# Kernel tuning notes

Measured on AMD Instinct MI355X. Metric: run time of the kernel, lower is better.

## Reference

```python
import jax, jax.numpy as jnp
import numpy as np

B, N, D, ATT = 8, 2048, 1024, 128

def setup_inputs() -> dict:
    key = jax.random.key(0)
    k1, k2, k3 = jax.random.split(key, 3)
    s = 1.0 / np.sqrt(D)
    return {
        "x": jax.random.normal(k1, (B, N, D), dtype=jnp.float32),
        "Wf": jax.random.normal(k2, (D, ATT), dtype=jnp.float32) * s,
        "bf": jnp.zeros((ATT,), dtype=jnp.float32),
        "Wg": jax.random.normal(k3, (D, ATT), dtype=jnp.float32) * s,
        "bg": jnp.zeros((ATT,), dtype=jnp.float32),
    }

def reference(x, Wf, bf, Wg, bg):
    # f, g: [B, N, ATT]
    f = jnp.einsum('bnd,da->bna', x, Wf) + bf
    g = jnp.einsum('bnd,da->bna', x, Wg) + bg
    # unscaled attention logits [B, N, N]
    att = jnp.einsum('bna,bma->bnm', f, g)
    att = jax.nn.softmax(att, axis=-1)
    # NOTE: original multiplies attention with x (not h); h branch is dead code.
    out = jnp.einsum('bnm,bmd->bnd', att, x)
    return out + x  # residual=True
```

## Files before the change

### kernel.cpp

```cpp
#include <hip/hip_runtime.h>
#include <hip/hip_fp16.h>


#define B_ 8
#define N_ 2048
#define D_ 1024
#define A_ 128

typedef _Float16 half8v  __attribute__((ext_vector_type(8)));
typedef _Float16 half4v  __attribute__((ext_vector_type(4)));
typedef short    short8v __attribute__((ext_vector_type(8)));
typedef float    floatx4 __attribute__((ext_vector_type(4)));

#define SOFT_C 44.0f

__device__ __forceinline__ floatx4 mfma32(half8v a, half8v b, floatx4 c) {
#if defined(__HIP_DEVICE_COMPILE__)
    return __builtin_amdgcn_mfma_f32_16x16x32_f16(a, b, c, 0, 0, 0);
#else
    return c;
#endif
}
__device__ __forceinline__ floatx4 mfma32bf(short8v a, short8v b, floatx4 c) {
#if defined(__HIP_DEVICE_COMPILE__)
    return __builtin_amdgcn_mfma_f32_16x16x32_bf16(a, b, c, 0, 0, 0);
#else
    return c;
#endif
}

__device__ __forceinline__ unsigned short f2bf(float x) {
    union { float f; unsigned int u; } v; v.f = x;
    unsigned int u = v.u + 0x7fffu + ((v.u >> 16) & 1u);
    return (unsigned short)(u >> 16);
}

__device__ __forceinline__ void gload_lds16(const void* gsrc, void* ldst) {
#if defined(__HIP_DEVICE_COMPILE__)
    __builtin_amdgcn_global_load_lds(
        (const __attribute__((address_space(1))) void*)gsrc,
        (__attribute__((address_space(3))) void*)ldst, 16, 0, 0);
#endif
}

__global__ __launch_bounds__(256) void xpose_kernel(
    const float* __restrict__ x, unsigned short* __restrict__ xT)
{
    __shared__ __align__(16) unsigned short ts[64][80];
    const int n0 = blockIdx.x * 64, d0 = blockIdx.y * 64, b = blockIdx.z;
    const int t = threadIdx.x;
#pragma unroll
    for (int s = 0; s < 4; ++s) {
        int idx = t + 256 * s;
        int nl = idx >> 4, c4 = idx & 15;
        float4 v = ((const float4*)(x + ((size_t)(b * N_ + n0 + nl)) * D_ + d0))[c4];
        ts[c4 * 4 + 0][nl] = f2bf(v.x);
        ts[c4 * 4 + 1][nl] = f2bf(v.y);
        ts[c4 * 4 + 2][nl] = f2bf(v.z);
        ts[c4 * 4 + 3][nl] = f2bf(v.w);
    }
    __syncthreads();
#pragma unroll
    for (int s = 0; s < 2; ++s) {
        int idx = t + 256 * s;
        int dl = idx >> 3, c = idx & 7;
        *(uint4*)&xT[((size_t)b * D_ + d0 + dl) * N_ + n0 + c * 8] =
            *(const uint4*)&ts[dl][c * 8];
    }
}

__global__ __launch_bounds__(256) void wprep_kernel(
    const float* __restrict__ Wf, const float* __restrict__ Wg,
    _Float16* __restrict__ whT)
{
    __shared__ __align__(16) _Float16 ts[64][72];
    const int k0 = blockIdx.x * 64, c0 = blockIdx.y * 64;
    const float* W = blockIdx.z ? Wg : Wf;
    _Float16* dst = whT + (size_t)blockIdx.z * A_ * D_;
    const int t = threadIdx.x;
#pragma unroll
    for (int s = 0; s < 4; ++s) {
        int idx = t + 256 * s;
        int kl = idx >> 4, c4 = idx & 15;
        float4 v = *(const float4*)&W[(size_t)(k0 + kl) * A_ + c0 + c4 * 4];
        ts[c4 * 4 + 0][kl] = (_Float16)v.x;
        ts[c4 * 4 + 1][kl] = (_Float16)v.y;
        ts[c4 * 4 + 2][kl] = (_Float16)v.z;
        ts[c4 * 4 + 3][kl] = (_Float16)v.w;
    }
    __syncthreads();
#pragma unroll
    for (int s = 0; s < 2; ++s) {
        int idx = t + 256 * s;
        int cl = idx >> 3, ch = idx & 7;
        *(uint4*)&dst[(size_t)(c0 + cl) * D_ + k0 + ch * 8] =
            *(const uint4*)&ts[cl][ch * 8];
    }
}

__global__ __launch_bounds__(256) void fgmm_kernel(
    const float* __restrict__ x, const _Float16* __restrict__ whT,
    const float* __restrict__ bfv, const float* __restrict__ bgv,
    _Float16* __restrict__ fh, _Float16* __restrict__ gh)
{
    __shared__ __align__(16) _Float16 xs[64 * 40];
    __shared__ __align__(16) _Float16 wt[256 * 40];
    const int row0 = blockIdx.x * 64;
    const int t = threadIdx.x;
    const int w = t >> 6, lane = t & 63, quad = lane >> 4, l16 = lane & 15;
    const int wr  = (w >> 1) * 32;
    const int wch = (w & 1);

    float4 xRf[2];
    uint4  wR[4];
#define FG_LOAD_TILE(K0)                                                      \
    {                                                                         \
        _Pragma("unroll")                                                     \
        for (int s = 0; s < 2; ++s) {                                         \
            int idx = t + 256 * s;                                            \
            int r = idx >> 3, k4 = idx & 7;                                   \
            xRf[s] = *(const float4*)&x[(size_t)(row0 + r) * D_ + (K0) + k4 * 4]; \
        }                                                                     \
        _Pragma("unroll")                                                     \
        for (int s = 0; s < 4; ++s) {                                         \
            int idx = t + 256 * s;                                            \
            int c = idx >> 2, k8 = idx & 3;                                   \
            wR[s] = *(const uint4*)&whT[(size_t)c * D_ + (K0) + k8 * 8];      \
        }                                                                     \
    }

    FG_LOAD_TILE(0)

    floatx4 acc[2][8];
#pragma unroll
    for (int ms = 0; ms < 2; ++ms)
#pragma unroll
        for (int nt = 0; nt < 8; ++nt)
            acc[ms][nt] = (floatx4){0.f, 0.f, 0.f, 0.f};

    for (int kt = 0; kt < 32; ++kt) {
        __syncthreads();
#pragma unroll
        for (int s = 0; s < 2; ++s) {
            int idx = t + 256 * s;
            int r = idx >> 3, k4 = idx & 7;
            half4v h = {(_Float16)xRf[s].x, (_Float16)xRf[s].y,
                        (_Float16)xRf[s].z, (_Float16)xRf[s].w};
            *(half4v*)&xs[r * 40 + k4 * 4] = h;
        }
#pragma unroll
        for (int s = 0; s < 4; ++s) {
            int idx = t + 256 * s;
            int c = idx >> 2, k8 = idx & 3;
            *(uint4*)&wt[c * 40 + k8 * 8] = wR[s];
        }
        __syncthreads();
        if (kt < 31) FG_LOAD_TILE((kt + 1) * 32)

        half8v a0 = *(const half8v*)&xs[(wr + l16) * 40 + quad * 8];
        half8v a1 = *(const half8v*)&xs[(wr + 16 + l16) * 40 + quad * 8];
#pragma unroll
        for (int nt = 0; nt < 8; ++nt) {
            half8v bfr = *(const half8v*)&wt[(wch * 128 + nt * 16 + l16) * 40 + quad * 8];
            acc[0][nt] = mfma32(a0, bfr, acc[0][nt]);
            acc[1][nt] = mfma32(a1, bfr, acc[1][nt]);
        }
    }

    _Float16* dst = wch ? gh : fh;
    const float* bias = wch ? bgv : bfv;
#pragma unroll
    for (int nt = 0; nt < 8; ++nt) {
        int col = nt * 16 + l16;
        float bv = bias[col];
#pragma unroll
        for (int ms = 0; ms < 2; ++ms)
#pragma unroll
            for (int rg = 0; rg < 4; ++rg) {
                int row = row0 + wr + ms * 16 + quad * 4 + rg;
                dst[(size_t)row * A_ + col] = (_Float16)(acc[ms][nt][rg] + bv);
            }
    }
}

__global__ __launch_bounds__(512) void attp_kernel(
    const _Float16* __restrict__ f, const _Float16* __restrict__ g,
    unsigned short* __restrict__ P, float* __restrict__ lsum)
{
    __shared__ __align__(16) unsigned short tps[8][16 * 56];
    __shared__ float lred[8][16];

    const int tid = threadIdx.x;
    const int wave = tid >> 6, lane = tid & 63;
    const int quad = lane >> 4, l16 = lane & 15;
    const int gp = wave >> 2, qg = wave & 3;
    const int q0 = blockIdx.x * 64;
    const int b  = blockIdx.y;

    half8v fb[4];
#pragma unroll
    for (int kc = 0; kc < 4; ++kc)
        fb[kc] = *(const half8v*)(f +
            ((size_t)(b * N_ + q0 + qg * 16 + l16)) * A_ + kc * 32 + quad * 8);

    unsigned short* slab = &tps[wave][0];
    float l_part = 0.f;

    for (int t = 0; t < 32; ++t) {
        const int m0 = gp * 1024 + t * 32;
        half8v ga0[4], ga1[4];
#pragma unroll
        for (int kc = 0; kc < 4; ++kc) {
            ga0[kc] = *(const half8v*)(g +
                ((size_t)(b * N_ + m0 + l16)) * A_ + kc * 32 + quad * 8);
            ga1[kc] = *(const half8v*)(g +
                ((size_t)(b * N_ + m0 + 16 + l16)) * A_ + kc * 32 + quad * 8);
        }
        floatx4 sc0 = (floatx4){0.f, 0.f, 0.f, 0.f};
        floatx4 sc1 = (floatx4){0.f, 0.f, 0.f, 0.f};
#pragma unroll
        for (int kc = 0; kc < 4; ++kc) {
            sc0 = mfma32(ga0[kc], fb[kc], sc0);
            sc1 = mfma32(ga1[kc], fb[kc], sc1);
        }
        float e0 = __expf(sc0[0] - SOFT_C), e1 = __expf(sc0[1] - SOFT_C);
        float e2 = __expf(sc0[2] - SOFT_C), e3 = __expf(sc0[3] - SOFT_C);
        float e4 = __expf(sc1[0] - SOFT_C), e5 = __expf(sc1[1] - SOFT_C);
        float e6 = __expf(sc1[2] - SOFT_C), e7 = __expf(sc1[3] - SOFT_C);
        l_part += ((e0 + e1) + (e2 + e3)) + ((e4 + e5) + (e6 + e7));
        unsigned int w01 = (unsigned int)f2bf(e0) | ((unsigned int)f2bf(e1) << 16);
        unsigned int w23 = (unsigned int)f2bf(e2) | ((unsigned int)f2bf(e3) << 16);
        unsigned int w45 = (unsigned int)f2bf(e4) | ((unsigned int)f2bf(e5) << 16);
        unsigned int w67 = (unsigned int)f2bf(e6) | ((unsigned int)f2bf(e7) << 16);
        *(unsigned int*)&slab[l16 * 56 + quad * 4]          = w01;
        *(unsigned int*)&slab[l16 * 56 + quad * 4 + 2]      = w23;
        *(unsigned int*)&slab[l16 * 56 + 16 + quad * 4]     = w45;
        *(unsigned int*)&slab[l16 * 56 + 16 + quad * 4 + 2] = w67;
        asm volatile("s_waitcnt lgkmcnt(0)" ::: "memory");
        __builtin_amdgcn_sched_barrier(0);
        uint4 pvv = *(const uint4*)&slab[(lane >> 2) * 56 + (lane & 3) * 8];
        *(uint4*)(P + ((size_t)(b * N_ + q0 + qg * 16 + (lane >> 2))) * N_ +
                  m0 + (lane & 3) * 8) = pvv;
    }

    l_part += __shfl_xor(l_part, 16);
    l_part += __shfl_xor(l_part, 32);
    if (lane < 16) lred[wave][lane] = l_part;
    __syncthreads();
    if (wave < 4 && lane < 16)
        lsum[(size_t)b * N_ + q0 + wave * 16 + lane] =
            lred[wave][lane] + lred[wave + 4][lane];
}

__global__ __launch_bounds__(256, 4) void pv_kernel(
    const unsigned short* __restrict__ P, const unsigned short* __restrict__ xT,
    const float* __restrict__ lsum, const float* __restrict__ x,
    float* __restrict__ out)
{
    __shared__ __align__(16) unsigned short Ps[2][128 * 32];
    __shared__ __align__(16) unsigned short Xs[2][128 * 32];

    const int bm = blockIdx.x;
    const int dn = blockIdx.y;
    const int b  = blockIdx.z;
    const int tid = threadIdx.x;
    const int wave = tid >> 6, lane = tid & 63;
    const int quad = lane >> 4, l16 = lane & 15;
    const int wm = wave >> 1, wn = wave & 1;
    const int xorv = (l16 >> 1) & 3;
    const int chq = (quad ^ xorv) * 8;

#define PV_STAGE(BUF, T0)                                                     \
    {                                                                         \
        _Pragma("unroll")                                                     \
        for (int s = 0; s < 2; ++s) {                                         \
            int idx = s * 256 + tid;                                          \
            int row = idx >> 2, c = idx & 3;                                  \
            int cc = c ^ ((row >> 1) & 3);                                    \
            gload_lds16(P + ((size_t)(b * N_ + bm * 128 + row)) * N_ +        \
                            (T0) + cc * 8,                                    \
                        &Ps[BUF][(s * 256 + wave * 64) * 8]);                 \
        }                                                                     \
        _Pragma("unroll")                                                     \
        for (int s = 0; s < 2; ++s) {                                         \
            int idx = s * 256 + tid;                                          \
            int row = idx >> 2, c = idx & 3;                                  \
            int cc = c ^ ((row >> 1) & 3);                                    \
            gload_lds16(xT + ((size_t)(b * D_ + dn * 128 + row)) * N_ +       \
                            (T0) + cc * 8,                                    \
                        &Xs[BUF][(s * 256 + wave * 64) * 8]);                 \
        }                                                                     \
    }

    floatx4 acc[4][4];
#pragma unroll
    for (int m = 0; m < 4; ++m)
#pragma unroll
        for (int n = 0; n < 4; ++n)
            acc[m][n] = (floatx4){0.f, 0.f, 0.f, 0.f};

    PV_STAGE(0, 0)
    __syncthreads();

    for (int t = 0; t < 64; ++t) {
        const int cur = t & 1;
        if (t < 63) PV_STAGE(cur ^ 1, (t + 1) * 32)

        short8v a[4], bb[4];
#pragma unroll
        for (int m = 0; m < 4; ++m)
            a[m] = *(const short8v*)&Ps[cur][(wm * 64 + m * 16 + l16) * 32 + chq];
#pragma unroll
        for (int n = 0; n < 4; ++n)
            bb[n] = *(const short8v*)&Xs[cur][(wn * 64 + n * 16 + l16) * 32 + chq];

        __builtin_amdgcn_s_setprio(1);
#pragma unroll
        for (int m = 0; m < 4; ++m)
#pragma unroll
            for (int n = 0; n < 4; ++n)
                acc[m][n] = mfma32bf(a[m], bb[n], acc[m][n]);
        __builtin_amdgcn_s_setprio(0);

        __syncthreads();
    }

    float linv[4][4];
#pragma unroll
    for (int m = 0; m < 4; ++m)
#pragma unroll
        for (int rg = 0; rg < 4; ++rg) {
            int row = bm * 128 + wm * 64 + m * 16 + quad * 4 + rg;
            linv[m][rg] = 1.0f / lsum[(size_t)b * N_ + row];
        }
#pragma unroll
    for (int m = 0; m < 4; ++m)
#pragma unroll
        for (int rg = 0; rg < 4; ++rg) {
            int row = bm * 128 + wm * 64 + m * 16 + quad * 4 + rg;
            const size_t rowoff = ((size_t)(b * N_ + row)) * D_ + dn * 128;
#pragma unroll
            for (int n = 0; n < 4; ++n) {
                int col = wn * 64 + n * 16 + l16;
                out[rowoff + col] =
                    fmaf(acc[m][n][rg], linv[m][rg], x[rowoff + col]);
            }
        }
}

extern "C" void kernel_launch(void* const* d_in, const int* in_sizes, int n_in,
                              void* d_out, int out_size, void* d_ws, size_t ws_size,
                              hipStream_t stream) {
    const float* x   = (const float*)d_in[0];
    const float* Wf  = (const float*)d_in[1];
    const float* bfv = (const float*)d_in[2];
    const float* Wg  = (const float*)d_in[3];
    const float* bgv = (const float*)d_in[4];
    float* out = (float*)d_out;

    _Float16*       fh  = (_Float16*)d_ws;
    _Float16*       gh  = fh + (size_t)B_ * N_ * A_;
    unsigned short* xT  = (unsigned short*)(gh + (size_t)B_ * N_ * A_);
    _Float16*       whT = (_Float16*)(xT + (size_t)B_ * D_ * N_);
    unsigned short* P   = (unsigned short*)(whT + (size_t)2 * A_ * D_);
    float*          lsum = (float*)(P + (size_t)B_ * N_ * N_);

    hipLaunchKernelGGL(xpose_kernel, dim3(N_ / 64, D_ / 64, B_), dim3(256), 0, stream,
                       x, xT);
    hipLaunchKernelGGL(wprep_kernel, dim3(D_ / 64, A_ / 64, 2), dim3(256), 0, stream,
                       Wf, Wg, whT);
    hipLaunchKernelGGL(fgmm_kernel, dim3(B_ * N_ / 64), dim3(256), 0, stream,
                       x, whT, bfv, bgv, fh, gh);
    hipLaunchKernelGGL(attp_kernel, dim3(N_ / 64, B_), dim3(512), 0, stream,
                       fh, gh, P, lsum);
    hipLaunchKernelGGL(pv_kernel, dim3(N_ / 128, D_ / 128, B_), dim3(256), 0, stream,
                       P, xT, lsum, x, out);
}
```

Baseline: 321.7 us.

## Triple-buffer PV loads with vmcnt waits and re-split attention-P grid

The pv_kernel moves from double to triple buffering of LDS tiles. It prefetches two stages ahead and replaces __syncthreads with explicit vmcnt/lgkmcnt waits plus s_barrier, so global loads overlap more with MFMA work. The attp_kernel now uses 256-thread blocks covering 16 query rows, with each wave handling a 512-key slice, and software-prefetches g tiles with ping-pong registers. In exchange it uses more LDS in pv_kernel, lowers its occupancy hint to 3, and launches more attp blocks.

Result: slower. 339.4 us (+5.5%).

```diff
diff --git a/kernel.cpp b/kernel.cpp
--- a/kernel.cpp
+++ b/kernel.cpp
@@ -183,82 +183,96 @@
     }
 }
 
-__global__ __launch_bounds__(512) void attp_kernel(
+__global__ __launch_bounds__(256) void attp_kernel(
     const _Float16* __restrict__ f, const _Float16* __restrict__ g,
     unsigned short* __restrict__ P, float* __restrict__ lsum)
 {
-    __shared__ __align__(16) unsigned short tps[8][16 * 56];
-    __shared__ float lred[8][16];
+    __shared__ __align__(16) unsigned short tps[4][16 * 56];
+    __shared__ float lred[4][16];
 
     const int tid = threadIdx.x;
     const int wave = tid >> 6, lane = tid & 63;
     const int quad = lane >> 4, l16 = lane & 15;
-    const int gp = wave >> 2, qg = wave & 3;
-    const int q0 = blockIdx.x * 64;
+    const int q0 = blockIdx.x * 16;
     const int b  = blockIdx.y;
+    const int kbase = wave * 512;
 
     half8v fb[4];
 #pragma unroll
     for (int kc = 0; kc < 4; ++kc)
         fb[kc] = *(const half8v*)(f +
-            ((size_t)(b * N_ + q0 + qg * 16 + l16)) * A_ + kc * 32 + quad * 8);
+            ((size_t)(b * N_ + q0 + l16)) * A_ + kc * 32 + quad * 8);
 
     unsigned short* slab = &tps[wave][0];
     float l_part = 0.f;
 
-    for (int t = 0; t < 32; ++t) {
-        const int m0 = gp * 1024 + t * 32;
-        half8v ga0[4], ga1[4];
-#pragma unroll
-        for (int kc = 0; kc < 4; ++kc) {
-            ga0[kc] = *(const half8v*)(g +
-                ((size_t)(b * N_ + m0 + l16)) * A_ + kc * 32 + quad * 8);
-            ga1[kc] = *(const half8v*)(g +
-                ((size_t)(b * N_ + m0 + 16 + l16)) * A_ + kc * 32 + quad * 8);
-        }
-        floatx4 sc0 = (floatx4){0.f, 0.f, 0.f, 0.f};
-        floatx4 sc1 = (floatx4){0.f, 0.f, 0.f, 0.f};
-#pragma unroll
-        for (int kc = 0; kc < 4; ++kc) {
-            sc0 = mfma32(ga0[kc], fb[kc], sc0);
-            sc1 = mfma32(ga1[kc], fb[kc], sc1);
-        }
-        float e0 = __expf(sc0[0] - SOFT_C), e1 = __expf(sc0[1] - SOFT_C);
-        float e2 = __expf(sc0[2] - SOFT_C), e3 = __expf(sc0[3] - SOFT_C);
-        float e4 = __expf(sc1[0] - SOFT_C), e5 = __expf(sc1[1] - SOFT_C);
-        float e6 = __expf(sc1[2] - SOFT_C), e7 = __expf(sc1[3] - SOFT_C);
-        l_part += ((e0 + e1) + (e2 + e3)) + ((e4 + e5) + (e6 + e7));
-        unsigned int w01 = (unsigned int)f2bf(e0) | ((unsigned int)f2bf(e1) << 16);
-        unsigned int w23 = (unsigned int)f2bf(e2) | ((unsigned int)f2bf(e3) << 16);
-        unsigned int w45 = (unsigned int)f2bf(e4) | ((unsigned int)f2bf(e5) << 16);
-        unsigned int w67 = (unsigned int)f2bf(e6) | ((unsigned int)f2bf(e7) << 16);
-        *(unsigned int*)&slab[l16 * 56 + quad * 4]          = w01;
-        *(unsigned int*)&slab[l16 * 56 + quad * 4 + 2]      = w23;
-        *(unsigned int*)&slab[l16 * 56 + 16 + quad * 4]     = w45;
-        *(unsigned int*)&slab[l16 * 56 + 16 + quad * 4 + 2] = w67;
-        asm volatile("s_waitcnt lgkmcnt(0)" ::: "memory");
-        __builtin_amdgcn_sched_barrier(0);
-        uint4 pvv = *(const uint4*)&slab[(lane >> 2) * 56 + (lane & 3) * 8];
-        *(uint4*)(P + ((size_t)(b * N_ + q0 + qg * 16 + (lane >> 2))) * N_ +
-                  m0 + (lane & 3) * 8) = pvv;
+#define ATTP_LOADG(A0, A1, M0)                                                \
+    {                                                                         \
+        _Pragma("unroll")                                                     \
+        for (int kc = 0; kc < 4; ++kc) {                                      \
+            A0[kc] = *(const half8v*)(g +                                     \
+                ((size_t)(b * N_ + (M0) + l16)) * A_ + kc * 32 + quad * 8);   \
+            A1[kc] = *(const half8v*)(g +                                     \
+                ((size_t)(b * N_ + (M0) + 16 + l16)) * A_ + kc * 32 + quad * 8); \
+        }                                                                     \
+    }
+
+#define ATTP_COMPUTE(A0, A1, TT)                                              \
+    {                                                                         \
+        const int m0 = kbase + (TT) * 32;                                     \
+        floatx4 sc0 = (floatx4){0.f, 0.f, 0.f, 0.f};                          \
+        floatx4 sc1 = (floatx4){0.f, 0.f, 0.f, 0.f};                          \
+        _Pragma("unroll")                                                     \
+        for (int kc = 0; kc < 4; ++kc) {                                      \
+            sc0 = mfma32(A0[kc], fb[kc], sc0);                                \
+            sc1 = mfma32(A1[kc], fb[kc], sc1);                                \
+        }                                                                     \
+        float e0 = __expf(sc0[0] - SOFT_C), e1 = __expf(sc0[1] - SOFT_C);     \
+        float e2 = __expf(sc0[2] - SOFT_C), e3 = __expf(sc0[3] - SOFT_C);     \
+        float e4 = __expf(sc1[0] - SOFT_C), e5 = __expf(sc1[1] - SOFT_C);     \
+        float e6 = __expf(sc1[2] - SOFT_C), e7 = __expf(sc1[3] - SOFT_C);     \
+        l_part += ((e0 + e1) + (e2 + e3)) + ((e4 + e5) + (e6 + e7));          \
+        unsigned int w01 = (unsigned int)f2bf(e0) | ((unsigned int)f2bf(e1) << 16); \
+        unsigned int w23 = (unsigned int)f2bf(e2) | ((unsigned int)f2bf(e3) << 16); \
+        unsigned int w45 = (unsigned int)f2bf(e4) | ((unsigned int)f2bf(e5) << 16); \
+        unsigned int w67 = (unsigned int)f2bf(e6) | ((unsigned int)f2bf(e7) << 16); \
+        *(unsigned int*)&slab[l16 * 56 + quad * 4]          = w01;            \
+        *(unsigned int*)&slab[l16 * 56 + quad * 4 + 2]      = w23;            \
+        *(unsigned int*)&slab[l16 * 56 + 16 + quad * 4]     = w45;            \
+        *(unsigned int*)&slab[l16 * 56 + 16 + quad * 4 + 2] = w67;            \
+        asm volatile("s_waitcnt lgkmcnt(0)" ::: "memory");                    \
+        __builtin_amdgcn_sched_barrier(0);                                    \
+        uint4 pvv = *(const uint4*)&slab[(lane >> 2) * 56 + (lane & 3) * 8];  \
+        *(uint4*)(P + ((size_t)(b * N_ + q0 + (lane >> 2))) * N_ +            \
+                  m0 + (lane & 3) * 8) = pvv;                                 \
+    }
+
+    half8v ga0[4], ga1[4], gb0[4], gb1[4];
+    ATTP_LOADG(ga0, ga1, kbase)
+#pragma unroll 1
+    for (int tp = 0; tp < 8; ++tp) {
+        ATTP_LOADG(gb0, gb1, kbase + (tp * 2 + 1) * 32)
+        ATTP_COMPUTE(ga0, ga1, tp * 2)
+        if (tp < 7) ATTP_LOADG(ga0, ga1, kbase + (tp * 2 + 2) * 32)
+        ATTP_COMPUTE(gb0, gb1, tp * 2 + 1)
     }
 
     l_part += __shfl_xor(l_part, 16);
     l_part += __shfl_xor(l_part, 32);
     if (lane < 16) lred[wave][lane] = l_part;
     __syncthreads();
-    if (wave < 4 && lane < 16)
-        lsum[(size_t)b * N_ + q0 + wave * 16 + lane] =
-            lred[wave][lane] + lred[wave + 4][lane];
-}
-
-__global__ __launch_bounds__(256, 4) void pv_kernel(
+    if (wave == 0 && lane < 16)
+        lsum[(size_t)b * N_ + q0 + lane] =
+            (lred[0][lane] + lred[1][lane]) + (lred[2][lane] + lred[3][lane]);
+}
+
+__global__ __launch_bounds__(256, 3) void pv_kernel(
     const unsigned short* __restrict__ P, const unsigned short* __restrict__ xT,
     const float* __restrict__ lsum, const float* __restrict__ x,
     float* __restrict__ out)
 {
-    __shared__ __align__(16) unsigned short Ps[2][128 * 32];
-    __shared__ __align__(16) unsigned short Xs[2][128 * 32];
+    __shared__ __align__(16) unsigned short Ps[3][128 * 32];
+    __shared__ __align__(16) unsigned short Xs[3][128 * 32];
 
     const int bm = blockIdx.x;
     const int dn = blockIdx.y;
@@ -300,11 +314,15 @@
             acc[m][n] = (floatx4){0.f, 0.f, 0.f, 0.f};
 
     PV_STAGE(0, 0)
-    __syncthreads();
-
+    PV_STAGE(1, 32)
+    asm volatile("s_waitcnt vmcnt(4)" ::: "memory");
+    __builtin_amdgcn_sched_barrier(0);
+    __builtin_amdgcn_s_barrier();
+
+    int cur = 0;
     for (int t = 0; t < 64; ++t) {
-        const int cur = t & 1;
-        if (t < 63) PV_STAGE(cur ^ 1, (t + 1) * 32)
+        int nx2 = cur + 2; if (nx2 >= 3) nx2 -= 3;
+        if (t < 62) PV_STAGE(nx2, (t + 2) * 32)
 
         short8v a[4], bb[4];
 #pragma unroll
@@ -322,7 +340,18 @@
                 acc[m][n] = mfma32bf(a[m], bb[n], acc[m][n]);
         __builtin_amdgcn_s_setprio(0);
 
-        __syncthreads();
+        if (t < 63) {
+            asm volatile("s_waitcnt lgkmcnt(0)" ::: "memory");
+            if (t < 62) {
+                asm volatile("s_waitcnt vmcnt(4)" ::: "memory");
+            } else {
+                asm volatile("s_waitcnt vmcnt(0)" ::: "memory");
+            }
+            __builtin_amdgcn_sched_barrier(0);
+            __builtin_amdgcn_s_barrier();
+            __builtin_amdgcn_sched_barrier(0);
+        }
+        cur = (cur == 2) ? 0 : cur + 1;
     }
 
     float linv[4][4];
@@ -371,7 +400,7 @@
                        Wf, Wg, whT);
     hipLaunchKernelGGL(fgmm_kernel, dim3(B_ * N_ / 64), dim3(256), 0, stream,
                        x, whT, bfv, bgv, fh, gh);
-    hipLaunchKernelGGL(attp_kernel, dim3(N_ / 64, B_), dim3(512), 0, stream,
+    hipLaunchKernelGGL(attp_kernel, dim3(N_ / 16, B_), dim3(256), 0, stream,
                        fh, gh, P, lsum);
     hipLaunchKernelGGL(pv_kernel, dim3(N_ / 128, D_ / 128, B_), dim3(256), 0, stream,
                        P, xT, lsum, x, out);
```
